# Optimization experiments

Measured on AMD Instinct MI355X. Metric: run time of the kernel, lower is better.

Reference implementation:

```python
import jax, jax.numpy as jnp
import numpy as np
import math

NG, NP, NC = 300, 100000, 80
ALPHA, BETA = 0.75, 1.0
K_MAX, K_MIN = 10, 1
EPS = 1e-7


def k_schedule(epoch, total_epochs):
    t = epoch / max(1, total_epochs - 1)
    K = int(round(K_MAX - (K_MAX - K_MIN) * t))
    return max(K_MIN, min(K_MAX, K))


def setup_inputs() -> dict:
    key = jax.random.key(0)
    k1, k2, k3 = jax.random.split(key, 3)
    preds = jax.random.normal(k1, (NP, 5 + NC), dtype=jnp.float32)
    gt_boxes = jax.random.uniform(k2, (NG, 4), dtype=jnp.float32)
    gt_classes = jax.random.randint(k3, (NG,), 0, NC, dtype=jnp.int32)
    return {"preds": preds, "gt_boxes": gt_boxes, "gt_classes": gt_classes,
            "epoch": 0, "total_epochs": 300}


def _cost_matrix(preds, gt_boxes, gt_classes):
    # preds: [Np, 5+C] (xywh, obj, cls_logits); gt_boxes: [Ng, 4] xyxy
    xc, yc, w, h = preds[:, 0], preds[:, 1], preds[:, 2], preds[:, 3]
    p = jnp.stack([xc - w / 2, yc - h / 2, xc + w / 2, yc + h / 2], axis=-1)  # [Np,4] xyxy
    g = gt_boxes  # [Ng,4]

    p_ = p[None, :, :]   # [1,Np,4]
    g_ = g[:, None, :]   # [Ng,1,4]

    # IoU  (bbox_iou with ci=pred, cj=gt)
    x1 = jnp.maximum(p_[..., 0], g_[..., 0])
    y1 = jnp.maximum(p_[..., 1], g_[..., 1])
    x2 = jnp.minimum(p_[..., 2], g_[..., 2])
    y2 = jnp.minimum(p_[..., 3], g_[..., 3])
    inter = jnp.clip(x2 - x1, 0) * jnp.clip(y2 - y1, 0)          # [Ng,Np]
    area_p = jnp.clip(p[:, 2] - p[:, 0], 0) * jnp.clip(p[:, 3] - p[:, 1], 0)   # [Np]
    area_g = jnp.clip(g[:, 2] - g[:, 0], 0) * jnp.clip(g[:, 3] - g[:, 1], 0)   # [Ng]
    union = area_p[None, :] + area_g[:, None] - inter + EPS
    iou = inter / union

    # center distance
    pcx = (p[:, 0] + p[:, 2]) / 2; pcy = (p[:, 1] + p[:, 3]) / 2   # [Np]
    gcx = (g[:, 0] + g[:, 2]) / 2; gcy = (g[:, 1] + g[:, 3]) / 2   # [Ng]
    center_dist2 = (pcx[None, :] - gcx[:, None]) ** 2 + (pcy[None, :] - gcy[:, None]) ** 2

    # enclosing box diagonal
    c_w = jnp.clip(jnp.maximum(p_[..., 2], g_[..., 2]) - jnp.minimum(p_[..., 0], g_[..., 0]), EPS)
    c_h = jnp.clip(jnp.maximum(p_[..., 3], g_[..., 3]) - jnp.minimum(p_[..., 1], g_[..., 1]), EPS)
    c2 = c_w ** 2 + c_h ** 2 + EPS

    # aspect-ratio term
    wp = jnp.clip(p[:, 2] - p[:, 0], EPS); hp = jnp.clip(p[:, 3] - p[:, 1], EPS)  # [Np]
    wg = jnp.clip(g[:, 2] - g[:, 0], EPS); hg = jnp.clip(g[:, 3] - g[:, 1], EPS)  # [Ng]
    v = (4.0 / math.pi ** 2) * (jnp.arctan(wg / hg)[:, None] - jnp.arctan(wp / hp)[None, :]) ** 2
    alpha_t = jax.lax.stop_gradient(v / ((1.0 - iou) + v + EPS))   # torch.no_grad block
    ciou = iou - center_dist2 / c2 - alpha_t * v                   # [Ng,Np] (= 1 - ciou_loss)

    # classification score for each pred at its gt's class
    cls_prob = jax.nn.sigmoid(preds[:, 5:])                        # [Np,C]
    cls_score = jnp.take(cls_prob, gt_classes, axis=1).T           # [Ng,Np]

    cost = ALPHA * (1.0 - cls_score) + BETA * (1.0 - jnp.clip(ciou, 0.0, 1.0))
    return cost


def reference(preds, gt_boxes, gt_classes, epoch, total_epochs):
    Ng, Np = gt_boxes.shape[0], preds.shape[0]
    Kt = min(k_schedule(epoch, total_epochs), Np)
    cost = _cost_matrix(preds, gt_boxes, gt_classes)               # [Ng,Np]
    _, topk_idx = jax.lax.top_k(-cost, Kt)                         # [Ng,Kt] smallest cost per gt
    gt_idx = jnp.broadcast_to(jnp.arange(Ng, dtype=topk_idx.dtype)[:, None], topk_idx.shape)
    assignments = jnp.stack([topk_idx.reshape(-1), gt_idx.reshape(-1)], axis=1)  # [Ng*Kt,2]
    return cost, assignments
```

## Files before the change

### kernel.cpp

```cpp
#include <hip/hip_runtime.h>
#include <math.h>

#define NG 300
#define NP 100000
#define NC 80
#define PRED_COLS 85
#define ALPHA_C 0.75f
#define BETA_C  1.0f
#define EPS_C   1e-7f
#define TPB 256
#define NBLK ((NP + TPB - 1) / TPB)
#define KCAP 10
#define NSLAB 20
#define GSLAB (NG / NSLAB)

__device__ __forceinline__ float fast_rcp(float x) {
    return __builtin_amdgcn_rcpf(x);
}

__device__ __forceinline__ float wave_min(float v) {
#pragma unroll
    for (int off = 32; off >= 1; off >>= 1)
        v = fminf(v, __shfl_xor(v, off));
    return v;
}

__device__ __forceinline__ void wave_lexmin(float& v, int& i) {
#pragma unroll
    for (int off = 32; off >= 1; off >>= 1) {
        float ov = __shfl_xor(v, off);
        int   oi = __shfl_xor(i, off);
        if (ov < v || (ov == v && oi < i)) { v = ov; i = oi; }
    }
}

__global__ __launch_bounds__(TPB) void prep_kernel(
    const float* __restrict__ preds, float* __restrict__ probs,
    float4* __restrict__ bA, float4* __restrict__ bB)
{
    int p = blockIdx.x * TPB + threadIdx.x;
    if (p >= NP) return;
    const float* row = preds + (size_t)p * PRED_COLS;
    if (blockIdx.y == 0) {
        float xc = row[0], yc = row[1], w = row[2], h = row[3];
        float px1 = xc - w * 0.5f, py1 = yc - h * 0.5f;
        float px2 = xc + w * 0.5f, py2 = yc + h * 0.5f;
        float4 a = {px1, py1, px2, py2};
        float4 b;
        b.x = fmaxf(px2 - px1, 0.f) * fmaxf(py2 - py1, 0.f);
        b.y = (px1 + px2) * 0.5f;
        b.z = (py1 + py2) * 0.5f;
        b.w = atanf(fmaxf(px2 - px1, EPS_C) / fmaxf(py2 - py1, EPS_C));
        bA[p] = a; bB[p] = b;
#pragma unroll
        for (int c = 0; c < 40; ++c)
            probs[(size_t)c * NP + p] = fast_rcp(1.f + expf(-row[5 + c]));
    } else {
#pragma unroll
        for (int c = 40; c < 80; ++c)
            probs[(size_t)c * NP + p] = fast_rcp(1.f + expf(-row[5 + c]));
    }
}

template <bool USE_PACK>
__global__ __launch_bounds__(TPB) void cost_kernel(
    const float* __restrict__ preds, const float* __restrict__ gt_boxes,
    const int* __restrict__ gt_classes, float* __restrict__ cost,
    const float* __restrict__ probs,
    const float4* __restrict__ bA, const float4* __restrict__ bB,
    float* __restrict__ mins)
{
    __shared__ float4 sbox[GSLAB];
    __shared__ float4 smisc[GSLAB];
    __shared__ int    scls[GSLAB];
    __shared__ float  swmin[4][GSLAB];

    const int g0 = blockIdx.y * GSLAB;
    const int lane = threadIdx.x & 63;
    const int wid  = threadIdx.x >> 6;

    for (int i = threadIdx.x; i < GSLAB; i += TPB) {
        int g = g0 + i;
        float4 b = ((const float4*)gt_boxes)[g];
        float x1 = b.x, y1 = b.y, x2 = b.z, y2 = b.w;
        sbox[i] = b;
        float4 m;
        m.x = fmaxf(x2 - x1, 0.f) * fmaxf(y2 - y1, 0.f);
        m.y = (x1 + x2) * 0.5f;
        m.z = (y1 + y2) * 0.5f;
        m.w = atanf(fmaxf(x2 - x1, EPS_C) / fmaxf(y2 - y1, EPS_C));
        smisc[i] = m;
        scls[i] = USE_PACK ? gt_classes[g] * NP : gt_classes[g];
    }
    __syncthreads();

    const int p = blockIdx.x * TPB + threadIdx.x;
    const bool valid = p < NP;
    const int pc = valid ? p : NP - 1;

    float px1, py1, px2, py2, areap, pcx, pcy, atp;
    const float* row = preds + (size_t)pc * PRED_COLS;
    if (USE_PACK) {
        float4 a = bA[pc], b = bB[pc];
        px1 = a.x; py1 = a.y; px2 = a.z; py2 = a.w;
        areap = b.x; pcx = b.y; pcy = b.z; atp = b.w;
    } else {
        float xc = row[0], yc = row[1], w = row[2], h = row[3];
        px1 = xc - w * 0.5f; py1 = yc - h * 0.5f;
        px2 = xc + w * 0.5f; py2 = yc + h * 0.5f;
        areap = fmaxf(px2 - px1, 0.f) * fmaxf(py2 - py1, 0.f);
        pcx = (px1 + px2) * 0.5f; pcy = (py1 + py2) * 0.5f;
        atp = atanf(fmaxf(px2 - px1, EPS_C) / fmaxf(py2 - py1, EPS_C));
    }

    float prob[GSLAB];
#pragma unroll
    for (int i = 0; i < GSLAB; ++i) {
        if (USE_PACK) prob[i] = probs[(size_t)scls[i] + pc];
        else          prob[i] = fast_rcp(1.f + expf(-row[5 + scls[i]]));
    }

    const float VC = (float)(4.0 / (M_PI * M_PI));
    float* out = cost + (size_t)g0 * NP + p;
    float mn[GSLAB];

#pragma unroll
    for (int i = 0; i < GSLAB; ++i) {
        float4 b = sbox[i];
        float4 m = smisc[i];
        float gx1 = b.x, gy1 = b.y, gx2 = b.z, gy2 = b.w;
        float xx1 = fmaxf(px1, gx1), yy1 = fmaxf(py1, gy1);
        float xx2 = fminf(px2, gx2), yy2 = fminf(py2, gy2);
        float inter = fmaxf(xx2 - xx1, 0.f) * fmaxf(yy2 - yy1, 0.f);
        float uni = areap + m.x - inter + EPS_C;
        float iou = inter * fast_rcp(uni);
        float dx = pcx - m.y, dy = pcy - m.z;
        float cd2 = dx * dx + dy * dy;
        float cw = fmaxf(fmaxf(px2, gx2) - fminf(px1, gx1), EPS_C);
        float ch = fmaxf(fmaxf(py2, gy2) - fminf(py1, gy1), EPS_C);
        float c2 = cw * cw + ch * ch + EPS_C;
        float dat = m.w - atp;
        float v = VC * dat * dat;
        float alpha_t = v * fast_rcp(1.f - iou + v + EPS_C);
        float ciou = iou - cd2 * fast_rcp(c2) - alpha_t * v;

        float cst = ALPHA_C * (1.f - prob[i]) +
                    BETA_C * (1.f - fminf(fmaxf(ciou, 0.f), 1.f));
        mn[i] = valid ? cst : INFINITY;
        if (valid) out[(size_t)i * NP] = cst;
    }

#pragma unroll
    for (int i = 0; i < GSLAB; ++i) {
        float v = wave_min(mn[i]);
        if (lane == 0) swmin[wid][i] = v;
    }
    __syncthreads();
    if (threadIdx.x < GSLAB) {
        int t = threadIdx.x;
        float v = fminf(fminf(swmin[0][t], swmin[1][t]),
                        fminf(swmin[2][t], swmin[3][t]));
        mins[(size_t)(g0 + t) * NBLK + blockIdx.x] = v;
    }
}

__global__ __launch_bounds__(TPB) void topk_fused(
    const float* __restrict__ cost, const float* __restrict__ mins,
    const int* __restrict__ epoch, const int* __restrict__ total_epochs,
    float* __restrict__ out_assign)
{
    const int g = blockIdx.x;
    const int lane = threadIdx.x & 63;
    const int wid  = threadIdx.x >> 6;

    __shared__ float s_thr;
    __shared__ int   s_qn;
    __shared__ int   qlist[NBLK];
    __shared__ float swv[4 * KCAP];
    __shared__ int   swi[4 * KCAP];

    if (threadIdx.x == 0) s_qn = 0;
    __syncthreads();

    const float* mrow = mins + (size_t)g * NBLK;

    if (wid == 0) {
        float v[7];
#pragma unroll
        for (int j = 0; j < 7; ++j) {
            int idx = lane + j * 64;
            v[j] = (idx < NBLK) ? mrow[idx] : INFINITY;
        }
        float last = INFINITY;
        for (int k = 0; k < KCAP; ++k) {
            float lm = v[0];
#pragma unroll
            for (int j = 1; j < 7; ++j) lm = fminf(lm, v[j]);
            float wv = lm; int wi = lane;
            wave_lexmin(wv, wi);
            last = wv;
            if (lane == wi) {
                bool done = false;
#pragma unroll
                for (int j = 0; j < 7; ++j)
                    if (!done && v[j] == lm) { v[j] = INFINITY; done = true; }
            }
        }
        if (lane == 0) s_thr = last;
    }
    __syncthreads();
    const float thr0 = s_thr;

    for (int b = threadIdx.x; b < NBLK; b += TPB)
        if (mrow[b] <= thr0) qlist[atomicAdd(&s_qn, 1)] = b;
    __syncthreads();
    const int qn = s_qn;

    float thr = thr0;
    float ev = INFINITY; int ei = 0x7fffffff;

    for (int qi = wid; qi < qn; qi += 4) {
        const int b = qlist[qi];
        const int ib = b * TPB + lane * 4;
        float vq[4];
        if (b == NBLK - 1) {
#pragma unroll
            for (int q = 0; q < 4; ++q)
                vq[q] = (ib + q < NP) ? cost[(size_t)g * NP + ib + q] : INFINITY;
        } else {
            float4 v = *(const float4*)(cost + (size_t)g * NP + ib);
            vq[0] = v.x; vq[1] = v.y; vq[2] = v.z; vq[3] = v.w;
        }
#pragma unroll
        for (int q = 0; q < 4; ++q) {
            unsigned long long m = __ballot(vq[q] <= thr);
            while (m) {
                int l = __ffsll(m) - 1;
                m &= m - 1;
                float cv = __shfl(vq[q], l);
                int   ci = __shfl(ib, l) + q;
                if (!(cv <= thr)) continue;
                bool prec = (ev < cv) || (ev == cv && ei < ci);
                unsigned long long bb = __ballot(prec) & 0x3FFull;
                int pos = __popcll(bb);
                if (pos < KCAP) {
                    float pev = __shfl_up(ev, 1);
                    int   pei = __shfl_up(ei, 1);
                    if (lane > pos && lane < KCAP) { ev = pev; ei = pei; }
                    if (lane == pos)               { ev = cv;  ei = ci;  }
                    thr = fminf(thr, __shfl(ev, KCAP - 1));
                }
            }
        }
    }

    if (lane < KCAP) { swv[wid * KCAP + lane] = ev; swi[wid * KCAP + lane] = ei; }
    __syncthreads();

    if (wid == 0) {
        float mv = (lane < 4 * KCAP) ? swv[lane] : INFINITY;
        int   mi = (lane < 4 * KCAP) ? swi[lane] : 0x7fffffff;

        int ep = epoch[0], te = total_epochs[0];
        int denom = te - 1; if (denom < 1) denom = 1;
        double tt = (double)ep / (double)denom;
        int K = (int)rint(10.0 - 9.0 * tt);
        if (K < 1) K = 1; if (K > 10) K = 10;
        int Kt = (K < NP) ? K : NP;

        for (int k = 0; k < Kt; ++k) {
            float wv = mv; int wi = mi;
            wave_lexmin(wv, wi);
            if (lane == 0) {
                out_assign[2 * ((size_t)g * Kt + k) + 0] = (float)wi;
                out_assign[2 * ((size_t)g * Kt + k) + 1] = (float)g;
            }
            if (mv == wv && mi == wi) { mv = INFINITY; mi = 0x7fffffff; }
        }
    }
}

extern "C" void kernel_launch(void* const* d_in, const int* in_sizes, int n_in,
                              void* d_out, int out_size, void* d_ws, size_t ws_size,
                              hipStream_t stream)
{
    const float* preds        = (const float*)d_in[0];
    const float* gt_boxes     = (const float*)d_in[1];
    const int*   gt_classes   = (const int*)d_in[2];
    const int*   epoch        = (const int*)d_in[3];
    const int*   total_epochs = (const int*)d_in[4];

    float* cost       = (float*)d_out;
    float* out_assign = cost + (size_t)NG * NP;

    size_t probBytes = (size_t)NC * NP * sizeof(float);
    size_t packBytes = (size_t)NP * 8 * sizeof(float);
    size_t minsBytes = (size_t)NG * NBLK * sizeof(float);

    char* wsp = (char*)d_ws;
    bool usePack = ws_size >= probBytes + packBytes + minsBytes;

    float *probs, *minsb; float4 *bA, *bB;
    if (usePack) {
        probs = (float*)wsp;
        bA    = (float4*)(wsp + probBytes);
        bB    = (float4*)(wsp + probBytes + packBytes / 2);
        minsb = (float*)(wsp + probBytes + packBytes);
    } else {
        probs = nullptr; bA = nullptr; bB = nullptr;
        minsb = (float*)wsp;
    }

    if (usePack) {
        prep_kernel<<<dim3(NBLK, 2), TPB, 0, stream>>>(preds, probs, bA, bB);
        cost_kernel<true ><<<dim3(NBLK, NSLAB), TPB, 0, stream>>>(
            preds, gt_boxes, gt_classes, cost, probs, bA, bB, minsb);
    } else {
        cost_kernel<false><<<dim3(NBLK, NSLAB), TPB, 0, stream>>>(
            preds, gt_boxes, gt_classes, cost, probs, bA, bB, minsb);
    }
    topk_fused<<<NG, TPB, 0, stream>>>(cost, minsb, epoch, total_epochs, out_assign);
}
```

Measured before the change: 221.3 us.

## Process four predictions per thread in cost kernel with float4 stores

Result: faster. 214.9 us (-2.9%).

```diff
diff --git a/kernel.cpp b/kernel.cpp
--- a/kernel.cpp
+++ b/kernel.cpp
@@ -9,7 +9,9 @@
 #define BETA_C  1.0f
 #define EPS_C   1e-7f
 #define TPB 256
-#define NBLK ((NP + TPB - 1) / TPB)
+#define VEC 4
+#define BLKP (TPB * VEC)
+#define NBLK4 ((NP + BLKP - 1) / BLKP)
 #define KCAP 10
 #define NSLAB 20
 #define GSLAB (NG / NSLAB)
@@ -94,65 +96,94 @@
     }
     __syncthreads();
 
-    const int p = blockIdx.x * TPB + threadIdx.x;
-    const bool valid = p < NP;
-    const int pc = valid ? p : NP - 1;
-
-    float px1, py1, px2, py2, areap, pcx, pcy, atp;
-    const float* row = preds + (size_t)pc * PRED_COLS;
-    if (USE_PACK) {
-        float4 a = bA[pc], b = bB[pc];
-        px1 = a.x; py1 = a.y; px2 = a.z; py2 = a.w;
-        areap = b.x; pcx = b.y; pcy = b.z; atp = b.w;
-    } else {
-        float xc = row[0], yc = row[1], w = row[2], h = row[3];
-        px1 = xc - w * 0.5f; py1 = yc - h * 0.5f;
-        px2 = xc + w * 0.5f; py2 = yc + h * 0.5f;
-        areap = fmaxf(px2 - px1, 0.f) * fmaxf(py2 - py1, 0.f);
-        pcx = (px1 + px2) * 0.5f; pcy = (py1 + py2) * 0.5f;
-        atp = atanf(fmaxf(px2 - px1, EPS_C) / fmaxf(py2 - py1, EPS_C));
-    }
-
-    float prob[GSLAB];
-#pragma unroll
-    for (int i = 0; i < GSLAB; ++i) {
-        if (USE_PACK) prob[i] = probs[(size_t)scls[i] + pc];
-        else          prob[i] = fast_rcp(1.f + expf(-row[5 + scls[i]]));
+    const int p0 = blockIdx.x * BLKP + threadIdx.x * VEC;
+    const bool full = (p0 + VEC - 1) < NP;
+
+    float px1[VEC], py1[VEC], px2[VEC], py2[VEC];
+    float areap[VEC], pcx[VEC], pcy[VEC], atp[VEC];
+    bool vld[VEC];
+#pragma unroll
+    for (int u = 0; u < VEC; ++u) {
+        int p = p0 + u;
+        vld[u] = p < NP;
+        int pc = vld[u] ? p : NP - 1;
+        if (USE_PACK) {
+            float4 a = bA[pc], b = bB[pc];
+            px1[u] = a.x; py1[u] = a.y; px2[u] = a.z; py2[u] = a.w;
+            areap[u] = b.x; pcx[u] = b.y; pcy[u] = b.z; atp[u] = b.w;
+        } else {
+            const float* row = preds + (size_t)pc * PRED_COLS;
+            float xc = row[0], yc = row[1], w = row[2], h = row[3];
+            px1[u] = xc - w * 0.5f; py1[u] = yc - h * 0.5f;
+            px2[u] = xc + w * 0.5f; py2[u] = yc + h * 0.5f;
+            areap[u] = fmaxf(px2[u] - px1[u], 0.f) * fmaxf(py2[u] - py1[u], 0.f);
+            pcx[u] = (px1[u] + px2[u]) * 0.5f; pcy[u] = (py1[u] + py2[u]) * 0.5f;
+            atp[u] = atanf(fmaxf(px2[u] - px1[u], EPS_C) / fmaxf(py2[u] - py1[u], EPS_C));
+        }
     }
 
     const float VC = (float)(4.0 / (M_PI * M_PI));
-    float* out = cost + (size_t)g0 * NP + p;
-    float mn[GSLAB];
 
 #pragma unroll
     for (int i = 0; i < GSLAB; ++i) {
         float4 b = sbox[i];
         float4 m = smisc[i];
         float gx1 = b.x, gy1 = b.y, gx2 = b.z, gy2 = b.w;
-        float xx1 = fmaxf(px1, gx1), yy1 = fmaxf(py1, gy1);
-        float xx2 = fminf(px2, gx2), yy2 = fminf(py2, gy2);
-        float inter = fmaxf(xx2 - xx1, 0.f) * fmaxf(yy2 - yy1, 0.f);
-        float uni = areap + m.x - inter + EPS_C;
-        float iou = inter * fast_rcp(uni);
-        float dx = pcx - m.y, dy = pcy - m.z;
-        float cd2 = dx * dx + dy * dy;
-        float cw = fmaxf(fmaxf(px2, gx2) - fminf(px1, gx1), EPS_C);
-        float ch = fmaxf(fmaxf(py2, gy2) - fminf(py1, gy1), EPS_C);
-        float c2 = cw * cw + ch * ch + EPS_C;
-        float dat = m.w - atp;
-        float v = VC * dat * dat;
-        float alpha_t = v * fast_rcp(1.f - iou + v + EPS_C);
-        float ciou = iou - cd2 * fast_rcp(c2) - alpha_t * v;
-
-        float cst = ALPHA_C * (1.f - prob[i]) +
-                    BETA_C * (1.f - fminf(fmaxf(ciou, 0.f), 1.f));
-        mn[i] = valid ? cst : INFINITY;
-        if (valid) out[(size_t)i * NP] = cst;
-    }
-
-#pragma unroll
-    for (int i = 0; i < GSLAB; ++i) {
-        float v = wave_min(mn[i]);
+
+        float pr[VEC];
+        if (USE_PACK) {
+            if (full) {
+                float4 pv = *(const float4*)(probs + (size_t)scls[i] + p0);
+                pr[0] = pv.x; pr[1] = pv.y; pr[2] = pv.z; pr[3] = pv.w;
+            } else {
+#pragma unroll
+                for (int u = 0; u < VEC; ++u)
+                    pr[u] = probs[(size_t)scls[i] + (vld[u] ? p0 + u : NP - 1)];
+            }
+        } else {
+#pragma unroll
+            for (int u = 0; u < VEC; ++u) {
+                int pc = vld[u] ? p0 + u : NP - 1;
+                pr[u] = fast_rcp(1.f + expf(-preds[(size_t)pc * PRED_COLS + 5 + scls[i]]));
+            }
+        }
+
+        float cst[VEC];
+#pragma unroll
+        for (int u = 0; u < VEC; ++u) {
+            float xx1 = fmaxf(px1[u], gx1), yy1 = fmaxf(py1[u], gy1);
+            float xx2 = fminf(px2[u], gx2), yy2 = fminf(py2[u], gy2);
+            float inter = fmaxf(xx2 - xx1, 0.f) * fmaxf(yy2 - yy1, 0.f);
+            float uni = areap[u] + m.x - inter + EPS_C;
+            float iou = inter * fast_rcp(uni);
+            float dx = pcx[u] - m.y, dy = pcy[u] - m.z;
+            float cd2 = dx * dx + dy * dy;
+            float cw = fmaxf(fmaxf(px2[u], gx2) - fminf(px1[u], gx1), EPS_C);
+            float ch = fmaxf(fmaxf(py2[u], gy2) - fminf(py1[u], gy1), EPS_C);
+            float c2 = cw * cw + ch * ch + EPS_C;
+            float dat = m.w - atp[u];
+            float v = VC * dat * dat;
+            float alpha_t = v * fast_rcp(1.f - iou + v + EPS_C);
+            float ciou = iou - cd2 * fast_rcp(c2) - alpha_t * v;
+            cst[u] = ALPHA_C * (1.f - pr[u]) +
+                     BETA_C * (1.f - fminf(fmaxf(ciou, 0.f), 1.f));
+        }
+
+        float* orow = cost + (size_t)(g0 + i) * NP;
+        if (full) {
+            float4 o = {cst[0], cst[1], cst[2], cst[3]};
+            *(float4*)(orow + p0) = o;
+        } else {
+#pragma unroll
+            for (int u = 0; u < VEC; ++u)
+                if (vld[u]) orow[p0 + u] = cst[u];
+        }
+
+        float mn = INFINITY;
+#pragma unroll
+        for (int u = 0; u < VEC; ++u)
+            mn = fminf(mn, vld[u] ? cst[u] : INFINITY);
+        float v = wave_min(mn);
         if (lane == 0) swmin[wid][i] = v;
     }
     __syncthreads();
@@ -160,7 +191,7 @@
         int t = threadIdx.x;
         float v = fminf(fminf(swmin[0][t], swmin[1][t]),
                         fminf(swmin[2][t], swmin[3][t]));
-        mins[(size_t)(g0 + t) * NBLK + blockIdx.x] = v;
+        mins[(size_t)(g0 + t) * NBLK4 + blockIdx.x] = v;
     }
 }
 
@@ -175,35 +206,31 @@
 
     __shared__ float s_thr;
     __shared__ int   s_qn;
-    __shared__ int   qlist[NBLK];
+    __shared__ int   qlist[NBLK4];
     __shared__ float swv[4 * KCAP];
     __shared__ int   swi[4 * KCAP];
 
     if (threadIdx.x == 0) s_qn = 0;
     __syncthreads();
 
-    const float* mrow = mins + (size_t)g * NBLK;
+    const float* mrow = mins + (size_t)g * NBLK4;
 
     if (wid == 0) {
-        float v[7];
-#pragma unroll
-        for (int j = 0; j < 7; ++j) {
+        float v[2];
+#pragma unroll
+        for (int j = 0; j < 2; ++j) {
             int idx = lane + j * 64;
-            v[j] = (idx < NBLK) ? mrow[idx] : INFINITY;
+            v[j] = (idx < NBLK4) ? mrow[idx] : INFINITY;
         }
         float last = INFINITY;
         for (int k = 0; k < KCAP; ++k) {
-            float lm = v[0];
-#pragma unroll
-            for (int j = 1; j < 7; ++j) lm = fminf(lm, v[j]);
+            float lm = fminf(v[0], v[1]);
             float wv = lm; int wi = lane;
             wave_lexmin(wv, wi);
             last = wv;
             if (lane == wi) {
-                bool done = false;
-#pragma unroll
-                for (int j = 0; j < 7; ++j)
-                    if (!done && v[j] == lm) { v[j] = INFINITY; done = true; }
+                if (v[0] == lm) v[0] = INFINITY;
+                else            v[1] = INFINITY;
             }
         }
         if (lane == 0) s_thr = last;
@@ -211,25 +238,27 @@
     __syncthreads();
     const float thr0 = s_thr;
 
-    for (int b = threadIdx.x; b < NBLK; b += TPB)
+    for (int b = threadIdx.x; b < NBLK4; b += TPB)
         if (mrow[b] <= thr0) qlist[atomicAdd(&s_qn, 1)] = b;
     __syncthreads();
     const int qn = s_qn;
 
     float thr = thr0;
     float ev = INFINITY; int ei = 0x7fffffff;
-
-    for (int qi = wid; qi < qn; qi += 4) {
-        const int b = qlist[qi];
-        const int ib = b * TPB + lane * 4;
+    const float* crow = cost + (size_t)g * NP;
+
+    for (int si = wid; si < qn * 4; si += 4) {
+        const int b   = qlist[si >> 2];
+        const int sub = si & 3;
+        const int ib  = b * BLKP + sub * 256 + lane * 4;
         float vq[4];
-        if (b == NBLK - 1) {
+        if (ib + 3 < NP) {
+            float4 v = *(const float4*)(crow + ib);
+            vq[0] = v.x; vq[1] = v.y; vq[2] = v.z; vq[3] = v.w;
+        } else {
 #pragma unroll
             for (int q = 0; q < 4; ++q)
-                vq[q] = (ib + q < NP) ? cost[(size_t)g * NP + ib + q] : INFINITY;
-        } else {
-            float4 v = *(const float4*)(cost + (size_t)g * NP + ib);
-            vq[0] = v.x; vq[1] = v.y; vq[2] = v.z; vq[3] = v.w;
+                vq[q] = (ib + q < NP) ? crow[ib + q] : INFINITY;
         }
 #pragma unroll
         for (int q = 0; q < 4; ++q) {
@@ -295,7 +324,7 @@
 
     size_t probBytes = (size_t)NC * NP * sizeof(float);
     size_t packBytes = (size_t)NP * 8 * sizeof(float);
-    size_t minsBytes = (size_t)NG * NBLK * sizeof(float);
+    size_t minsBytes = (size_t)NG * NBLK4 * sizeof(float);
 
     char* wsp = (char*)d_ws;
     bool usePack = ws_size >= probBytes + packBytes + minsBytes;
@@ -311,12 +340,13 @@
         minsb = (float*)wsp;
     }
 
+    const int pblocks = (NP + TPB - 1) / TPB;
     if (usePack) {
-        prep_kernel<<<dim3(NBLK, 2), TPB, 0, stream>>>(preds, probs, bA, bB);
-        cost_kernel<true ><<<dim3(NBLK, NSLAB), TPB, 0, stream>>>(
+        prep_kernel<<<dim3(pblocks, 2), TPB, 0, stream>>>(preds, probs, bA, bB);
+        cost_kernel<true ><<<dim3(NBLK4, NSLAB), TPB, 0, stream>>>(
             preds, gt_boxes, gt_classes, cost, probs, bA, bB, minsb);
     } else {
-        cost_kernel<false><<<dim3(NBLK, NSLAB), TPB, 0, stream>>>(
+        cost_kernel<false><<<dim3(NBLK4, NSLAB), TPB, 0, stream>>>(
             preds, gt_boxes, gt_classes, cost, probs, bA, bB, minsb);
     }
     topk_fused<<<NG, TPB, 0, stream>>>(cost, minsb, epoch, total_epochs, out_assign);
```
